# Kernel tuning notes

Measured on AMD Instinct MI355X. Metric: run time of the kernel, lower is better.

## Reference

```python
import jax, jax.numpy as jnp
import numpy as np
from jax import lax

B, T, I, H, L = 64, 256, 512, 1024, 2


def setup_inputs() -> dict:
    key = jax.random.key(0)
    ks = jax.random.split(key, 6)
    s = 0.05  # small init scale for numerical stability
    return {
        "x": jax.random.normal(ks[0], (B, T, I), dtype=jnp.float32),
        "h0": jnp.zeros((L, B, H), dtype=jnp.float32),
        "c0": jnp.zeros((L, B, H), dtype=jnp.float32),
        "W_ih_0": jax.random.normal(ks[1], (I, 4 * H), dtype=jnp.float32) * s,
        "W_hh_0": jax.random.normal(ks[2], (H, 4 * H), dtype=jnp.float32) * s,
        "b_0": jnp.zeros((4 * H,), dtype=jnp.float32),
        "W_ih_1": jax.random.normal(ks[3], (H, 4 * H), dtype=jnp.float32) * s,
        "W_hh_1": jax.random.normal(ks[4], (H, 4 * H), dtype=jnp.float32) * s,
        "b_1": jnp.zeros((4 * H,), dtype=jnp.float32),
    }


def _lstm_layer(x_tbd, h0, c0, W_ih, W_hh, b):
    """x_tbd: [T, B, in]; returns ([T, B, H], h_T, c_T). Standard (Zaremba) LSTM cell."""
    def step(carry, xt):
        h, c = carry
        gates = xt @ W_ih + h @ W_hh + b  # [B, 4H]
        i, f, g, o = jnp.split(gates, 4, axis=-1)
        i = jax.nn.sigmoid(i)
        f = jax.nn.sigmoid(f)
        g = jnp.tanh(g)
        o = jax.nn.sigmoid(o)
        c_new = f * c + i * g
        h_new = o * jnp.tanh(c_new)
        return (h_new, c_new), h_new

    (h_T, c_T), ys = lax.scan(step, (h0, c0), x_tbd)
    return ys, h_T, c_T


def reference(x, h0, c0, W_ih_0, W_hh_0, b_0, W_ih_1, W_hh_1, b_1):
    # x: [B, T, I] batch-first as in the torch module; scan over time.
    xt = jnp.swapaxes(x, 0, 1)  # [T, B, I]
    weights = [(W_ih_0, W_hh_0, b_0), (W_ih_1, W_hh_1, b_1)]
    hs, cs = [], []
    values = xt
    for l in range(L):
        W_ih, W_hh, b = weights[l]
        values, h_T, c_T = _lstm_layer(values, h0[l], c0[l], W_ih, W_hh, b)
        hs.append(h_T)
        cs.append(c_T)
    outputs = jnp.swapaxes(values, 0, 1)  # [B, T, H]
    return outputs, jnp.stack(hs, 0), jnp.stack(cs, 0)
```

## Files before the change

kernel.cpp:

```cpp
#include <hip/hip_runtime.h>
#include <hip/hip_bf16.h>

typedef __attribute__((ext_vector_type(8))) short short8;
typedef __attribute__((ext_vector_type(4))) float f32x4;

constexpr int BB = 64;
constexpr int TT = 256;
constexpr int II = 512;
constexpr int HH = 1024;

constexpr int NBLK = 256;
constexpr int NTHR = 512;

constexpr int HTILE = (HH / 8) * BB * 8;
constexpr int XTILE = (II / 8) * BB * 8;
constexpr int RING = 8;

constexpr size_t OFF_FLAGS = 0;
constexpr size_t OFF_WIH0T = 4096;
constexpr size_t OFF_WHH0T = OFF_WIH0T + (size_t)4096 * 512 * 2;
constexpr size_t OFF_WIH1T = OFF_WHH0T + (size_t)4096 * 1024 * 2;
constexpr size_t OFF_WHH1T = OFF_WIH1T + (size_t)4096 * 1024 * 2;
constexpr size_t OFF_XT    = OFF_WHH1T + (size_t)4096 * 1024 * 2;
constexpr size_t OFF_H0D   = OFF_XT + (size_t)TT * XTILE * 2;
constexpr size_t OFF_H1D   = OFF_H0D + (size_t)RING * HTILE * 2;

__device__ __forceinline__ float sigmoid_(float x) {
  return 1.f / (1.f + __expf(-x));
}
__device__ __forceinline__ float tanh_(float x) {
  float ax = fabsf(x);
  float e = __expf(-2.f * ax);
  float t = (1.f - e) / (1.f + e);
  return copysignf(t, x);
}

__global__ void zero_flags(int* f) { f[blockIdx.x * 256 + threadIdx.x] = 0; }

__global__ void transpose_to_bf16(const float* __restrict__ src,
                                  __hip_bfloat16* __restrict__ dst,
                                  int K, int N) {
  __shared__ float tile[64][65];
  const int n0 = blockIdx.x * 64;
  const int k0 = blockIdx.y * 64;
  const int tx = threadIdx.x & 63;
  const int ty = threadIdx.x >> 6;
#pragma unroll
  for (int i = 0; i < 64; i += 4)
    tile[ty + i][tx] = src[(size_t)(k0 + ty + i) * N + n0 + tx];
  __syncthreads();
#pragma unroll
  for (int i = 0; i < 64; i += 4) {
    const int n = ty + i;
    dst[(size_t)(n0 + n) * K + k0 + tx] = __float2bfloat16(tile[tx][n]);
  }
}

__global__ void tile_x(const float* __restrict__ x, __hip_bfloat16* __restrict__ xt) {
  const int t = blockIdx.x;
  const int k = threadIdx.x;
  __hip_bfloat16* o = xt + (size_t)t * XTILE;
  for (int b = 0; b < BB; ++b) {
    float v = x[((size_t)b * TT + t) * II + k];
    o[(k >> 3) * (BB * 8) + b * 8 + (k & 7)] = __float2bfloat16(v);
  }
}

__global__ void init_h(const float* __restrict__ h0, __hip_bfloat16* h0d, __hip_bfloat16* h1d) {
  const int idx = blockIdx.x * 256 + threadIdx.x;
  const int l = idx >> 16;
  const int b = (idx >> 10) & 63;
  const int j = idx & 1023;
  __hip_bfloat16 v = __float2bfloat16(h0[idx]);
  __hip_bfloat16* dst = l ? h1d : h0d;
  dst[(j >> 3) * (BB * 8) + b * 8 + (j & 7)] = v;
}

template <int LAYER>
__device__ __forceinline__ int chunk_kg(int wave, int c) {
  if constexpr (LAYER == 0)
    return (c < 2) ? (wave * 2 + c) * 32 : 512 + (wave * 4 + (c - 2)) * 32;
  else
    return (c < 4) ? (wave * 4 + c) * 32 : 1024 + (wave * 4 + (c - 4)) * 32;
}

template <int KI, int KW, int CA, int LAYER>
__device__ __forceinline__ void scan_impl(
    const __hip_bfloat16* __restrict__ xsrc,
    const __hip_bfloat16* __restrict__ WiT,
    const __hip_bfloat16* __restrict__ WhT,
    const float* __restrict__ bias,
    const float* __restrict__ c0_in,
    __hip_bfloat16* h0d, __hip_bfloat16* h1d,
    float* __restrict__ out, int* flags, float (*part)[2][4][4][65],
    int bhalf, int jbase) {
  const int tid = threadIdx.x;
  const int wave = tid >> 6;
  const int lane = tid & 63;
  const int cc = lane & 15;
  const int lrow = lane >> 4;

  short8 Bf[KW][4];
#pragma unroll
  for (int c = 0; c < KW; ++c) {
    const int kg = chunk_kg<LAYER>(wave, c) + lrow * 8;
#pragma unroll
    for (int g = 0; g < 4; ++g) {
      const int gcol = g * HH + jbase + cc;
      const __hip_bfloat16* p;
      if (kg < KI) p = WiT + (size_t)gcol * KI + kg;
      else         p = WhT + (size_t)gcol * HH + (kg - KI);
      Bf[c][g] = *(const short8*)p;
    }
  }

  const int ejl = tid & 15;
  const int ebl = tid >> 4;
  const int ej = jbase + ejl;
  const int eb = bhalf * 32 + ebl;
  const int pm = ebl >> 4, psub = (ebl >> 2) & 3, pr = ebl & 3;
  const int plane = psub * 16 + ejl;
  const float bi = bias[ej];
  const float bf_ = bias[HH + ej];
  const float bg = bias[2 * HH + ej];
  const float bo = bias[3 * HH + ej];
  float cst = c0_in[(size_t)LAYER * BB * HH + (size_t)eb * HH + ej];

  for (int tau = 0; tau < TT + 2; ++tau) {
    const bool active = (LAYER == 0) ? (tau < TT) : (tau >= 2);
    const int p = (LAYER == 0) ? tau : tau - 2;

    const __hip_bfloat16* px;
    const __hip_bfloat16* ph;
    __hip_bfloat16* hout;
    if constexpr (LAYER == 0) {
      px = xsrc + (size_t)p * XTILE;
      ph = h0d + (size_t)(p & (RING - 1)) * HTILE;
      hout = h0d + (size_t)((p + 1) & (RING - 1)) * HTILE;
    } else {
      px = h0d + (size_t)((p + 1) & (RING - 1)) * HTILE;
      ph = h1d + (size_t)(p & (RING - 1)) * HTILE;
      hout = h1d + (size_t)((p + 1) & (RING - 1)) * HTILE;
    }

    f32x4 acc[2][4] = {};
    short8 abuf[4][2];

    auto issue_chunk = [&](int c, short8* dst) {
      const int kg = chunk_kg<LAYER>(wave, c);
      const __hip_bfloat16* ab;
      int kc;
      if (kg < KI) { ab = px; kc = (kg >> 3) + lrow; }
      else         { ab = ph; kc = ((kg - KI) >> 3) + lrow; }
#pragma unroll
      for (int m = 0; m < 2; ++m) {
        const __hip_bfloat16* ptr =
            ab + (size_t)kc * (BB * 8) + (size_t)(bhalf * 32 + m * 16 + cc) * 8;
        asm volatile("global_load_dwordx4 %0, %1, off" : "=v"(dst[m]) : "v"(ptr));
      }
    };

    if (active) {
#pragma unroll
      for (int c = 0; c < CA; ++c) issue_chunk(c, abuf[c]);
    }

    if (tau > 0 && wave == 0) {
      for (;;) {
        int v0 = __hip_atomic_load(&flags[lane],       __ATOMIC_RELAXED, __HIP_MEMORY_SCOPE_AGENT);
        int v1 = __hip_atomic_load(&flags[lane + 64],  __ATOMIC_RELAXED, __HIP_MEMORY_SCOPE_AGENT);
        int v2 = __hip_atomic_load(&flags[lane + 128], __ATOMIC_RELAXED, __HIP_MEMORY_SCOPE_AGENT);
        int v3 = __hip_atomic_load(&flags[lane + 192], __ATOMIC_RELAXED, __HIP_MEMORY_SCOPE_AGENT);
        int mn = min(min(v0, v1), min(v2, v3));
        if (__all(mn >= tau)) break;
        __builtin_amdgcn_s_sleep(2);
      }
    }

    if (active) {
      asm volatile("s_waitcnt vmcnt(0)" ::: "memory");
      __builtin_amdgcn_sched_barrier(0);
#pragma unroll
      for (int c = 0; c < CA; ++c)
#pragma unroll
        for (int m = 0; m < 2; ++m)
#pragma unroll
          for (int g = 0; g < 4; ++g)
            acc[m][g] = __builtin_amdgcn_mfma_f32_16x16x32_bf16(
                abuf[c][m], Bf[c][g], acc[m][g], 0, 0, 0);
    }

    __syncthreads();
    if (wave == 0)
      __builtin_amdgcn_fence(__ATOMIC_ACQUIRE, "agent");
    __syncthreads();

    if (active) {
      constexpr int NB = KW - CA;
#pragma unroll
      for (int c = 0; c < NB; ++c) issue_chunk(CA + c, abuf[c]);
#pragma unroll
      for (int c = 0; c < NB; ++c) {
        const int vm = 2 * (NB - 1 - c);
        if (vm == 6)      asm volatile("s_waitcnt vmcnt(6)" ::: "memory");
        else if (vm == 4) asm volatile("s_waitcnt vmcnt(4)" ::: "memory");
        else if (vm == 2) asm volatile("s_waitcnt vmcnt(2)" ::: "memory");
        else              asm volatile("s_waitcnt vmcnt(0)" ::: "memory");
        __builtin_amdgcn_sched_barrier(0);
#pragma unroll
        for (int m = 0; m < 2; ++m)
#pragma unroll
          for (int g = 0; g < 4; ++g)
            acc[m][g] = __builtin_amdgcn_mfma_f32_16x16x32_bf16(
                abuf[c][m], Bf[CA + c][g], acc[m][g], 0, 0, 0);
      }

#pragma unroll
      for (int m = 0; m < 2; ++m)
#pragma unroll
        for (int g = 0; g < 4; ++g)
#pragma unroll
          for (int r = 0; r < 4; ++r)
            part[wave][m][g][r][lane] = acc[m][g][r];
      __syncthreads();

      float s0 = 0.f, s1 = 0.f, s2 = 0.f, s3 = 0.f;
#pragma unroll
      for (int w = 0; w < 8; ++w) {
        s0 += part[w][pm][0][pr][plane];
        s1 += part[w][pm][1][pr][plane];
        s2 += part[w][pm][2][pr][plane];
        s3 += part[w][pm][3][pr][plane];
      }
      float iv = sigmoid_(s0 + bi);
      float fv = sigmoid_(s1 + bf_);
      float gv = tanh_(s2 + bg);
      float ov = sigmoid_(s3 + bo);
      float cn = fv * cst + iv * gv;
      cst = cn;
      float hv = ov * tanh_(cn);
      __hip_bfloat16 hb = __float2bfloat16(hv);
      unsigned short hu = *reinterpret_cast<unsigned short*>(&hb);
      unsigned pu = (unsigned)__shfl_xor((int)hu, 1);
      if ((tid & 1) == 0) {
        uint32_t packed = (uint32_t)hu | ((pu & 0xffffu) << 16);
        uint32_t* hq = (uint32_t*)hout;
        __hip_atomic_store(hq + (ej >> 3) * 256 + eb * 4 + ((ej & 7) >> 1), packed,
                           __ATOMIC_RELAXED, __HIP_MEMORY_SCOPE_AGENT);
      }
      asm volatile("s_waitcnt vmcnt(0)" ::: "memory");
      __syncthreads();
      if (tid == 0)
        __hip_atomic_store(&flags[blockIdx.x], tau + 1, __ATOMIC_RELAXED, __HIP_MEMORY_SCOPE_AGENT);
      if constexpr (LAYER == 1)
        out[((size_t)eb * TT + p) * HH + ej] = hv;
      if (p == TT - 1) {
        out[(size_t)BB * TT * HH + (size_t)LAYER * BB * HH + (size_t)eb * HH + ej] = hv;
        out[(size_t)BB * TT * HH + (size_t)2 * BB * HH + (size_t)LAYER * BB * HH + (size_t)eb * HH + ej] = cn;
      }
    } else {
      __syncthreads();
      if (tid == 0)
        __hip_atomic_store(&flags[blockIdx.x], tau + 1, __ATOMIC_RELAXED, __HIP_MEMORY_SCOPE_AGENT);
    }
  }
}

__global__ __launch_bounds__(NTHR, 2) void lstm_scan(
    const __hip_bfloat16* __restrict__ xt,
    const __hip_bfloat16* __restrict__ Wih0T, const __hip_bfloat16* __restrict__ Whh0T,
    const __hip_bfloat16* __restrict__ Wih1T, const __hip_bfloat16* __restrict__ Whh1T,
    const float* __restrict__ b0, const float* __restrict__ b1,
    const float* __restrict__ c0_in,
    __hip_bfloat16* h0d, __hip_bfloat16* h1d,
    float* __restrict__ out, int* flags) {
  __shared__ float part[8][2][4][4][65];
  const int blk = blockIdx.x;
  const int jslot = blk & 63;
  const int bhalf = (blk >> 6) & 1;
  const int jbase = jslot * 16;
  if ((blk >> 7) == 0)
    scan_impl<512, 6, 2, 0>(xt, Wih0T, Whh0T, b0, c0_in, h0d, h1d, out, flags, part, bhalf, jbase);
  else
    scan_impl<1024, 8, 4, 1>(nullptr, Wih1T, Whh1T, b1, c0_in, h0d, h1d, out, flags, part, bhalf, jbase);
}

extern "C" void kernel_launch(void* const* d_in, const int* in_sizes, int n_in,
                              void* d_out, int out_size, void* d_ws, size_t ws_size,
                              hipStream_t stream) {
  (void)in_sizes; (void)n_in; (void)out_size; (void)ws_size;
  const float* x    = (const float*)d_in[0];
  const float* h0   = (const float*)d_in[1];
  const float* c0   = (const float*)d_in[2];
  const float* Wih0 = (const float*)d_in[3];
  const float* Whh0 = (const float*)d_in[4];
  const float* b0   = (const float*)d_in[5];
  const float* Wih1 = (const float*)d_in[6];
  const float* Whh1 = (const float*)d_in[7];
  const float* b1   = (const float*)d_in[8];
  float* out = (float*)d_out;
  char* ws = (char*)d_ws;

  int* flags = (int*)(ws + OFF_FLAGS);
  __hip_bfloat16* wih0t = (__hip_bfloat16*)(ws + OFF_WIH0T);
  __hip_bfloat16* whh0t = (__hip_bfloat16*)(ws + OFF_WHH0T);
  __hip_bfloat16* wih1t = (__hip_bfloat16*)(ws + OFF_WIH1T);
  __hip_bfloat16* whh1t = (__hip_bfloat16*)(ws + OFF_WHH1T);
  __hip_bfloat16* xtl   = (__hip_bfloat16*)(ws + OFF_XT);
  __hip_bfloat16* h0d   = (__hip_bfloat16*)(ws + OFF_H0D);
  __hip_bfloat16* h1d   = (__hip_bfloat16*)(ws + OFF_H1D);

  zero_flags<<<2, 256, 0, stream>>>(flags);
  transpose_to_bf16<<<dim3(64, 8),  256, 0, stream>>>(Wih0, wih0t, 512, 4096);
  transpose_to_bf16<<<dim3(64, 16), 256, 0, stream>>>(Whh0, whh0t, 1024, 4096);
  transpose_to_bf16<<<dim3(64, 16), 256, 0, stream>>>(Wih1, wih1t, 1024, 4096);
  transpose_to_bf16<<<dim3(64, 16), 256, 0, stream>>>(Whh1, whh1t, 1024, 4096);
  tile_x<<<TT, 512, 0, stream>>>(x, xtl);
  init_h<<<512, 256, 0, stream>>>(h0, h0d, h1d);
  lstm_scan<<<NBLK, NTHR, 0, stream>>>(xtl, wih0t, whh0t, wih1t, whh1t,
                                       b0, b1, c0, h0d, h1d, out, flags);
}
```

Before: 1.618 ms.

## Replace the per-step acquire fence with buffer_inv, merge barriers and vectorize LDS partials

Each timestep now starts with a cache invalidate (buffer_inv sc0 sc1) in place of the agent-scope acquire fence that sat between two __syncthreads after the flag wait. That leaves a single barrier after the spin-wait. The second batch of activation loads is issued right after that barrier, and the first chunk's MFMAs run under a partial vmcnt(8) wait so they overlap the outstanding loads. The cross-wave partial-sum buffer in LDS now holds f32x4 values, written with vector stores and read through flat indices, with no padding. The risks are memory-ordering correctness, since the invalidate comes before the flag wait, and possible LDS bank conflicts from the unpadded layout.

New measurement: 4.349 ms. 169% more time.

```diff
diff --git a/kernel.cpp b/kernel.cpp
--- a/kernel.cpp
+++ b/kernel.cpp
@@ -92,13 +92,14 @@
     const float* __restrict__ bias,
     const float* __restrict__ c0_in,
     __hip_bfloat16* h0d, __hip_bfloat16* h1d,
-    float* __restrict__ out, int* flags, float (*part)[2][4][4][65],
+    float* __restrict__ out, int* flags, f32x4 (*part)[2][4][64],
     int bhalf, int jbase) {
   const int tid = threadIdx.x;
   const int wave = tid >> 6;
   const int lane = tid & 63;
   const int cc = lane & 15;
   const int lrow = lane >> 4;
+  constexpr int NB = KW - CA;
 
   short8 Bf[KW][4];
 #pragma unroll
@@ -119,7 +120,7 @@
   const int ej = jbase + ejl;
   const int eb = bhalf * 32 + ebl;
   const int pm = ebl >> 4, psub = (ebl >> 2) & 3, pr = ebl & 3;
-  const int plane = psub * 16 + ejl;
+  const int rdbase = pm * 1024 + (psub * 16 + ejl) * 4 + pr;
   const float bi = bias[ej];
   const float bf_ = bias[HH + ej];
   const float bg = bias[2 * HH + ej];
@@ -129,6 +130,8 @@
   for (int tau = 0; tau < TT + 2; ++tau) {
     const bool active = (LAYER == 0) ? (tau < TT) : (tau >= 2);
     const int p = (LAYER == 0) ? tau : tau - 2;
+
+    asm volatile("buffer_inv sc0 sc1" ::: "memory");
 
     const __hip_bfloat16* px;
     const __hip_bfloat16* ph;
@@ -144,7 +147,8 @@
     }
 
     f32x4 acc[2][4] = {};
-    short8 abuf[4][2];
+    short8 abufA[CA][2];
+    short8 abufB[NB][2];
 
     auto issue_chunk = [&](int c, short8* dst) {
       const int kg = chunk_kg<LAYER>(wave, c);
@@ -162,7 +166,7 @@
 
     if (active) {
 #pragma unroll
-      for (int c = 0; c < CA; ++c) issue_chunk(c, abuf[c]);
+      for (int c = 0; c < CA; ++c) issue_chunk(c, abufA[c]);
     }
 
     if (tau > 0 && wave == 0) {
@@ -176,61 +180,49 @@
         __builtin_amdgcn_s_sleep(2);
       }
     }
+    __syncthreads();
 
     if (active) {
+#pragma unroll
+      for (int c = 0; c < NB; ++c) issue_chunk(CA + c, abufB[c]);
+
+      asm volatile("s_waitcnt vmcnt(8)" ::: "memory");
+      __builtin_amdgcn_sched_barrier(0);
+#pragma unroll
+      for (int c = 0; c < CA; ++c)
+#pragma unroll
+        for (int m = 0; m < 2; ++m)
+#pragma unroll
+          for (int g = 0; g < 4; ++g)
+            acc[m][g] = __builtin_amdgcn_mfma_f32_16x16x32_bf16(
+                abufA[c][m], Bf[c][g], acc[m][g], 0, 0, 0);
+
       asm volatile("s_waitcnt vmcnt(0)" ::: "memory");
       __builtin_amdgcn_sched_barrier(0);
 #pragma unroll
-      for (int c = 0; c < CA; ++c)
+      for (int c = 0; c < NB; ++c)
 #pragma unroll
         for (int m = 0; m < 2; ++m)
 #pragma unroll
           for (int g = 0; g < 4; ++g)
             acc[m][g] = __builtin_amdgcn_mfma_f32_16x16x32_bf16(
-                abuf[c][m], Bf[c][g], acc[m][g], 0, 0, 0);
-    }
-
-    __syncthreads();
-    if (wave == 0)
-      __builtin_amdgcn_fence(__ATOMIC_ACQUIRE, "agent");
-    __syncthreads();
-
-    if (active) {
-      constexpr int NB = KW - CA;
-#pragma unroll
-      for (int c = 0; c < NB; ++c) issue_chunk(CA + c, abuf[c]);
-#pragma unroll
-      for (int c = 0; c < NB; ++c) {
-        const int vm = 2 * (NB - 1 - c);
-        if (vm == 6)      asm volatile("s_waitcnt vmcnt(6)" ::: "memory");
-        else if (vm == 4) asm volatile("s_waitcnt vmcnt(4)" ::: "memory");
-        else if (vm == 2) asm volatile("s_waitcnt vmcnt(2)" ::: "memory");
-        else              asm volatile("s_waitcnt vmcnt(0)" ::: "memory");
-        __builtin_amdgcn_sched_barrier(0);
-#pragma unroll
-        for (int m = 0; m < 2; ++m)
-#pragma unroll
-          for (int g = 0; g < 4; ++g)
-            acc[m][g] = __builtin_amdgcn_mfma_f32_16x16x32_bf16(
-                abuf[c][m], Bf[CA + c][g], acc[m][g], 0, 0, 0);
-      }
+                abufB[c][m], Bf[CA + c][g], acc[m][g], 0, 0, 0);
 
 #pragma unroll
       for (int m = 0; m < 2; ++m)
 #pragma unroll
         for (int g = 0; g < 4; ++g)
-#pragma unroll
-          for (int r = 0; r < 4; ++r)
-            part[wave][m][g][r][lane] = acc[m][g][r];
+          part[wave][m][g][lane] = acc[m][g];
       __syncthreads();
 
+      const float* pp = (const float*)part;
       float s0 = 0.f, s1 = 0.f, s2 = 0.f, s3 = 0.f;
 #pragma unroll
       for (int w = 0; w < 8; ++w) {
-        s0 += part[w][pm][0][pr][plane];
-        s1 += part[w][pm][1][pr][plane];
-        s2 += part[w][pm][2][pr][plane];
-        s3 += part[w][pm][3][pr][plane];
+        s0 += pp[w * 2048 + 0 * 256 + rdbase];
+        s1 += pp[w * 2048 + 1 * 256 + rdbase];
+        s2 += pp[w * 2048 + 2 * 256 + rdbase];
+        s3 += pp[w * 2048 + 3 * 256 + rdbase];
       }
       float iv = sigmoid_(s0 + bi);
       float fv = sigmoid_(s1 + bf_);
@@ -274,7 +266,7 @@
     const float* __restrict__ c0_in,
     __hip_bfloat16* h0d, __hip_bfloat16* h1d,
     float* __restrict__ out, int* flags) {
-  __shared__ float part[8][2][4][4][65];
+  __shared__ f32x4 part[8][2][4][64];
   const int blk = blockIdx.x;
   const int jslot = blk & 63;
   const int bhalf = (blk >> 6) & 1;
```
